# Performance work log

Measured on AMD Instinct MI355X. Metric: run time of the kernel, lower is better.

The kernel has to match this reference:

```python
import jax, jax.numpy as jnp
import numpy as np
from jax import lax

S = 2          # scale_factor
SS = S * S     # scale_factor ** 2 = groups = deform_groups
K = 3
KK = K * K
PAD = K // 2
EPS = 1e-5


def setup_inputs() -> dict:
    key = jax.random.key(0)
    k1, k2, k3, k4, k5, k6 = jax.random.split(key, 6)
    B, C, H, W = 2, 64, 128, 128
    Cin = C * SS            # 256, DCN input channels after repeat
    Cout = 64 * SS          # 256, DCN output channels
    x = jax.random.normal(k1, (B, C, H, W), jnp.float32)
    # small offset-branch weights so learned offsets stay within a few pixels
    w_offset = jax.random.normal(k2, (3 * SS * KK, Cin, K, K), jnp.float32) * 0.01
    b_offset = jax.random.normal(k3, (3 * SS * KK,), jnp.float32) * 0.01
    w_dcn = jax.random.normal(k4, (Cout, Cin // SS, K, K), jnp.float32) * (1.0 / np.sqrt((Cin // SS) * KK))
    gamma = jax.random.normal(k5, (64,), jnp.float32) * 0.1 + 1.0
    beta = jax.random.normal(k6, (64,), jnp.float32) * 0.1
    return {"x": x, "w_offset": w_offset, "b_offset": b_offset,
            "w_dcn": w_dcn, "gamma": gamma, "beta": beta}


def _deform_upsample(x, w_offset, b_offset, w_dcn, gamma, beta):
    B, C, H, W = x.shape
    xr = jnp.tile(x, (1, SS, 1, 1))            # [B, C*SS, H, W]
    Cin = C * SS
    dg = SS
    # ---- conv_offset branch (standard conv, pad=1) ----
    off = lax.conv_general_dilated(
        xr, w_offset, window_strides=(1, 1), padding=[(PAD, PAD), (PAD, PAD)],
        dimension_numbers=("NCHW", "OIHW", "NCHW"))
    off = off + b_offset[None, :, None, None]
    o1, o2, mask = jnp.split(off, 3, axis=1)
    offset = jnp.concatenate([o1, o2], axis=1).reshape(B, dg, KK, 2, H, W)
    dy = offset[:, :, :, 0]                    # [B, dg, KK, H, W]
    dx = offset[:, :, :, 1]
    mask = jax.nn.sigmoid(mask).reshape(B, dg, KK, H, W)
    # ---- deformable bilinear sampling ----
    kh = (jnp.arange(KK) // K - PAD).astype(jnp.float32)   # kernel tap row offsets
    kw = (jnp.arange(KK) % K - PAD).astype(jnp.float32)
    hh = jnp.arange(H, dtype=jnp.float32)
    ww = jnp.arange(W, dtype=jnp.float32)
    py = hh[None, :, None] + kh[:, None, None] + dy        # [B, dg, KK, H, W]
    px = ww[None, None, :] + kw[:, None, None] + dx
    y0f = jnp.floor(py)
    x0f = jnp.floor(px)
    ly = py - y0f
    lx = px - x0f
    y0 = y0f.astype(jnp.int32)
    x0 = x0f.astype(jnp.int32)
    Cg = Cin // dg
    xg = xr.reshape(B, dg, Cg, H * W)

    def gather(yi, xi):
        valid = (yi >= 0) & (yi < H) & (xi >= 0) & (xi < W)  # [B, dg, KK, H, W]
        yc = jnp.clip(yi, 0, H - 1)
        xc = jnp.clip(xi, 0, W - 1)
        idx = (yc * W + xc).reshape(B, dg, -1)               # [B, dg, KK*H*W]
        v = jax.vmap(jax.vmap(lambda xf, i: xf[:, i]))(xg, idx)  # [B, dg, Cg, KK*H*W]
        v = v.reshape(B, dg, Cg, KK, H, W)
        return v * valid[:, :, None].astype(v.dtype)

    w00 = (1 - ly) * (1 - lx)
    w01 = (1 - ly) * lx
    w10 = ly * (1 - lx)
    w11 = ly * lx
    col = (gather(y0, x0) * w00[:, :, None]
           + gather(y0, x0 + 1) * w01[:, :, None]
           + gather(y0 + 1, x0) * w10[:, :, None]
           + gather(y0 + 1, x0 + 1) * w11[:, :, None])       # [B, dg, Cg, KK, H, W]
    col = col * mask[:, :, None]
    # ---- grouped conv (groups == deform_groups, channel partitions coincide) ----
    Cout = w_dcn.shape[0]
    Cog = Cout // dg
    wg = w_dcn.reshape(dg, Cog, Cg, KK)
    y = jnp.einsum("bgcphw,gocp->bgohw", col, wg).reshape(B, Cout, H, W)
    # ---- channel reshuffle (pixel-shuffle style upsample) ----
    outc = Cout // SS
    y = y.reshape(B, S, S, outc, H, W).transpose(0, 3, 4, 1, 5, 2)
    y = y.reshape(B, outc, H * S, W * S)
    # ---- BatchNorm (batch stats, training mode) + ReLU ----
    mean = y.mean(axis=(0, 2, 3), keepdims=True)
    var = y.var(axis=(0, 2, 3), keepdims=True)
    y = (y - mean) * lax.rsqrt(var + EPS) * gamma[None, :, None, None] + beta[None, :, None, None]
    return jax.nn.relu(y)


def reference(x, w_offset, b_offset, w_dcn, gamma, beta):
    return _deform_upsample(x, w_offset, b_offset, w_dcn, gamma, beta)
```

## Files before the change

### kernel.cpp

```cpp
#include <hip/hip_runtime.h>
#include <hip/hip_bf16.h>
#include <math.h>

#define CH 64
#define HH 128
#define WW 128
#define HW 16384
#define NVALS 131072.f

#define STATS  0
#define BIAS2  256
#define WACONV 384
#define WADCN  32640
#define OACC   106368
#define XT     1875840
#define PARTS  2924416

typedef unsigned short ushort_t;
typedef unsigned int uint_t;
typedef __attribute__((ext_vector_type(8))) short bf16x8;
typedef __attribute__((ext_vector_type(4))) float f32x4;

__device__ __forceinline__ float bflo(uint_t u) { return __uint_as_float(u << 16); }
__device__ __forceinline__ float bfhi(uint_t u) { return __uint_as_float(u & 0xFFFF0000u); }
__device__ __forceinline__ float bfu(ushort_t s) { return __uint_as_float(((uint_t)s) << 16); }
__device__ __forceinline__ ushort_t f2bf(float f) {
    __hip_bfloat16 h = __float2bfloat16(f);
    return *(ushort_t*)&h;
}
__device__ __forceinline__ uint_t pack2(float lo, float hi) {
    return (uint_t)f2bf(lo) | ((uint_t)f2bf(hi) << 16);
}

__device__ __forceinline__ int off_chan(int g, int j) {
    return (j < 18) ? (g * 18 + j) : (72 + g * 9 + (j - 18));
}

__global__ void prep(const float* __restrict__ w_offset, const float* __restrict__ b_offset,
                     const float* __restrict__ w_dcn, float* __restrict__ ws) {
    int tid = blockIdx.x * 256 + threadIdx.x;
    if (tid < 64512) {
        int jp = tid & 7;
        int lane = (tid >> 3) & 63;
        int rest = tid >> 9;
        int mt = rest % 7;
        int kt = rest / 7;
        int m = mt * 16 + (lane & 15);
        int off = ((lane >> 4) << 3) + jp;
        int c = ((kt & 1) << 5) + off;
        int k = kt >> 1;
        float s = 0.f;
        if (m < 108) {
            int och = off_chan(m / 27, m % 27);
#pragma unroll
            for (int ss = 0; ss < 4; ++ss)
                s += w_offset[(och * 256 + ss * 64 + c) * 9 + k];
        }
        ((ushort_t*)(ws + WACONV))[tid] = f2bf(s);
    }
    if (tid < 147456) {
        int jp = tid & 7;
        int lane = (tid >> 3) & 63;
        int q = tid >> 9;
        int mt = q & 3;
        int kt = (q >> 2) % 18;
        int g = q / 72;
        int m = mt * 16 + (lane & 15);
        int c = ((kt & 1) << 5) + ((lane >> 4) << 3) + jp;
        int tap = kt >> 1;
        ((ushort_t*)(ws + WADCN))[tid] = f2bf(w_dcn[((g * 64 + m) * 64 + c) * 9 + tap]);
    }
    if (tid < 108) ws[BIAS2 + tid] = b_offset[off_chan(tid / 27, tid % 27)];
    if (tid < 128) ws[STATS + tid] = 0.f;
}

__global__ __launch_bounds__(256) void transpose_x(const float* __restrict__ x,
                                                   ushort_t* __restrict__ xT) {
    int b = blockIdx.x >> 8;
    int px0 = (blockIdx.x & 255) << 6;
    __shared__ float lds[64][65];
    int t = threadIdx.x;
    int lx = t & 63;
    int row = t >> 6;
    const float* xb = x + (size_t)b * CH * HW;
#pragma unroll
    for (int i = 0; i < 16; ++i) {
        int c = i * 4 + row;
        lds[c][lx] = xb[(size_t)c * HW + px0 + lx];
    }
    __syncthreads();
    ushort_t* dst = xT + ((size_t)b * HW + px0) * 64;
#pragma unroll
    for (int i = 0; i < 16; ++i) {
        int p = i * 4 + row;
        dst[(size_t)p * 64 + lx] = f2bf(lds[lx][p]);
    }
}

__global__ __launch_bounds__(256, 2) void conv_mfma(const ushort_t* __restrict__ xT,
                                                    const ushort_t* __restrict__ wA,
                                                    const float* __restrict__ biasM,
                                                    ushort_t* __restrict__ oaccb) {
    int blk = blockIdx.x;
    int b = blk >> 7;
    int tile = blk & 127;
    int th = tile >> 3, tw = tile & 7;
    int t = threadIdx.x;
    int wv = t >> 6, lane = t & 63;
    int lw = lane & 15, kg = lane >> 4;

    __shared__ ushort_t lds[180 * 72];

    const ushort_t* xTb = xT + (size_t)b * HW * 64;
    for (int rr = t; rr < 180; rr += 256) {
        int r = rr / 18, c2 = rr - r * 18;
        int hy = th * 8 + r - 1, wx = tw * 16 + c2 - 1;
        bool valid = (hy >= 0) && (hy < HH) && (wx >= 0) && (wx < WW);
        uint4* dst = (uint4*)&lds[rr * 72];
        if (valid) {
            const uint4* src = (const uint4*)(xTb + ((size_t)(hy * WW + wx)) * 64);
#pragma unroll
            for (int ch = 0; ch < 8; ++ch) dst[ch] = src[ch];
        } else {
            uint4 z; z.x = z.y = z.z = z.w = 0;
#pragma unroll
            for (int ch = 0; ch < 8; ++ch) dst[ch] = z;
        }
    }
    __syncthreads();

    f32x4 acc[7][2];
#pragma unroll
    for (int mt = 0; mt < 7; ++mt)
#pragma unroll
        for (int i = 0; i < 2; ++i)
            acc[mt][i] = (f32x4){0.f, 0.f, 0.f, 0.f};

    const bf16x8* wAv = (const bf16x8*)wA;
    for (int kt = 0; kt < 18; ++kt) {
        int k = kt >> 1;
        int dh = k / 3, dw = k - dh * 3;
        int hh = kt & 1;
        bf16x8 bfrag[2];
#pragma unroll
        for (int i = 0; i < 2; ++i) {
            int nt = wv * 2 + i;
            int rr = (nt + dh) * 18 + lw + dw;
            bfrag[i] = *(const bf16x8*)&lds[rr * 72 + ((hh << 2) + kg) * 8];
        }
        bf16x8 afrag[7];
#pragma unroll
        for (int mt = 0; mt < 7; ++mt)
            afrag[mt] = wAv[(kt * 7 + mt) * 64 + lane];
#pragma unroll
        for (int mt = 0; mt < 7; ++mt)
#pragma unroll
            for (int i = 0; i < 2; ++i)
                acc[mt][i] = __builtin_amdgcn_mfma_f32_16x16x32_bf16(
                    afrag[mt], bfrag[i], acc[mt][i], 0, 0, 0);
    }

#pragma unroll
    for (int mt = 0; mt < 7; ++mt) {
#pragma unroll
        for (int r = 0; r < 4; ++r) {
            int m = mt * 16 + (kg << 2) + r;
            if (m < 108) {
                float bia = biasM[m];
#pragma unroll
                for (int i = 0; i < 2; ++i) {
                    int hgl = th * 8 + wv * 2 + i;
                    int wgl = tw * 16 + lw;
                    oaccb[((size_t)b * 108 + m) * HW + hgl * WW + wgl] =
                        f2bf(acc[mt][i][r] + bia);
                }
            }
        }
    }
}

__global__ __launch_bounds__(256, 4) void dcn_mfma(const ushort_t* __restrict__ xT,
                                                   const ushort_t* __restrict__ oaccb,
                                                   const ushort_t* __restrict__ wA,
                                                   float* __restrict__ out) {
    int blk = blockIdx.x;
    int xcd = blk & 7;
    int b = xcd >> 2;
    int quad = xcd & 3;
    int unit = blk >> 3;
    int g = unit >> 5;
    int tl = unit & 31;
    int th = quad * 4 + (tl >> 3);
    int tw = tl & 7;
    int t = threadIdx.x;
    int wv = t >> 6, lane = t & 63;
    int lw = lane & 15, kg = lane >> 4;

    __shared__ ushort_t colLDS[128 * 72];
    __shared__ uint_t idxLDS[4][128];
    __shared__ float  wgtLDS[4][128];

    const ushort_t* xTb = xT + (size_t)b * HW * 64;

    int p1 = t & 127;
    int h1 = th * 8 + (p1 >> 4);
    int w1 = tw * 16 + (p1 & 15);
    const ushort_t* ob_in = oaccb + (size_t)(b * 4 + g) * 27 * HW + h1 * WW + w1;

    f32x4 acc[4][2];
#pragma unroll
    for (int mt = 0; mt < 4; ++mt)
#pragma unroll
        for (int i = 0; i < 2; ++i)
            acc[mt][i] = (f32x4){0.f, 0.f, 0.f, 0.f};

    const bf16x8* wAv = (const bf16x8*)wA + (size_t)g * 4608;

    for (int k = 0; k < 9; ++k) {
        if (t < 128) {
            float dy = bfu(ob_in[(size_t)(2 * k) * HW]);
            float dx = bfu(ob_in[(size_t)(2 * k + 1) * HW]);
            float mk = 1.f / (1.f + expf(-bfu(ob_in[(size_t)(18 + k) * HW])));

            float py = (float)h1 + (float)(k / 3 - 1) + dy;
            float qx = (float)w1 + (float)(k % 3 - 1) + dx;
            float y0f = floorf(py), x0f = floorf(qx);
            float ly = py - y0f, lx = qx - x0f;
            int y0 = (int)y0f, x0 = (int)x0f;
            int y1 = y0 + 1, x1 = x0 + 1;

            bool vy0 = (y0 >= 0) && (y0 < HH), vy1 = (y1 >= 0) && (y1 < HH);
            bool vx0 = (x0 >= 0) && (x0 < WW), vx1 = (x1 >= 0) && (x1 < WW);
            int yc0 = min(max(y0, 0), HH - 1), yc1 = min(max(y1, 0), HH - 1);
            int xc0 = min(max(x0, 0), WW - 1), xc1 = min(max(x1, 0), WW - 1);

            idxLDS[0][p1] = (uint_t)(yc0 * WW + xc0);
            idxLDS[1][p1] = (uint_t)(yc0 * WW + xc1);
            idxLDS[2][p1] = (uint_t)(yc1 * WW + xc0);
            idxLDS[3][p1] = (uint_t)(yc1 * WW + xc1);
            wgtLDS[0][p1] = (1.f - ly) * (1.f - lx) * mk * ((vy0 && vx0) ? 1.f : 0.f);
            wgtLDS[1][p1] = (1.f - ly) * lx * mk * ((vy0 && vx1) ? 1.f : 0.f);
            wgtLDS[2][p1] = ly * (1.f - lx) * mk * ((vy1 && vx0) ? 1.f : 0.f);
            wgtLDS[3][p1] = ly * lx * mk * ((vy1 && vx1) ? 1.f : 0.f);
        }
        __syncthreads();

        int chunk = t & 7;
#pragma unroll
        for (int iter = 0; iter < 4; ++iter) {
            int p = iter * 32 + (t >> 3);
            uint_t i00 = idxLDS[0][p], i01 = idxLDS[1][p];
            uint_t i10 = idxLDS[2][p], i11 = idxLDS[3][p];
            float w00 = wgtLDS[0][p], w01 = wgtLDS[1][p];
            float w10 = wgtLDS[2][p], w11 = wgtLDS[3][p];
            uint4 u00 = *(const uint4*)(xTb + (size_t)i00 * 64 + chunk * 8);
            uint4 u01 = *(const uint4*)(xTb + (size_t)i01 * 64 + chunk * 8);
            uint4 u10 = *(const uint4*)(xTb + (size_t)i10 * 64 + chunk * 8);
            uint4 u11 = *(const uint4*)(xTb + (size_t)i11 * 64 + chunk * 8);
            uint4 res;
#define CMB(E) pack2(w00 * bflo(u00.E) + w01 * bflo(u01.E) + w10 * bflo(u10.E) + w11 * bflo(u11.E), \
                     w00 * bfhi(u00.E) + w01 * bfhi(u01.E) + w10 * bfhi(u10.E) + w11 * bfhi(u11.E))
            res.x = CMB(x);
            res.y = CMB(y);
            res.z = CMB(z);
            res.w = CMB(w);
#undef CMB
            *(uint4*)&colLDS[p * 72 + chunk * 8] = res;
        }
        __syncthreads();

#pragma unroll
        for (int kt2 = 0; kt2 < 2; ++kt2) {
            int kt = k * 2 + kt2;
            bf16x8 bfrag[2];
#pragma unroll
            for (int i = 0; i < 2; ++i)
                bfrag[i] = *(const bf16x8*)
                    &colLDS[((wv * 2 + i) * 16 + lw) * 72 + (kt2 * 4 + kg) * 8];
            bf16x8 afrag[4];
#pragma unroll
            for (int mt = 0; mt < 4; ++mt)
                afrag[mt] = wAv[(kt * 4 + mt) * 64 + lane];
#pragma unroll
            for (int mt = 0; mt < 4; ++mt)
#pragma unroll
                for (int i = 0; i < 2; ++i)
                    acc[mt][i] = __builtin_amdgcn_mfma_f32_16x16x32_bf16(
                        afrag[mt], bfrag[i], acc[mt][i], 0, 0, 0);
        }
        __syncthreads();
    }

    int s1 = g >> 1, s2 = g & 1;
#pragma unroll
    for (int mt = 0; mt < 4; ++mt) {
#pragma unroll
        for (int i = 0; i < 2; ++i) {
            int p2 = (wv * 2 + i) * 16 + lw;
            int hg = th * 8 + (p2 >> 4);
            int wg = tw * 16 + (p2 & 15);
            float* op = out + ((size_t)b * 64 + mt * 16 + (kg << 2)) * 65536
                      + (size_t)(hg * 2 + s1) * 256 + (wg * 2 + s2);
#pragma unroll
            for (int r = 0; r < 4; ++r)
                op[(size_t)r * 65536] = acc[mt][i][r];
        }
    }
}

__global__ __launch_bounds__(256) void stats_sum(const float* __restrict__ out,
                                                 float* __restrict__ parts) {
    int o = blockIdx.x >> 2;
    int part = blockIdx.x & 3;
    int t = threadIdx.x;
    float s = 0.f, s2 = 0.f;
#pragma unroll
    for (int b = 0; b < 2; ++b) {
        const float* p = out + (size_t)b * 64 * 65536 + (size_t)o * 65536
                       + (size_t)part * 16384;
        for (int i = t * 4; i < 16384; i += 1024) {
            float4 v = *(const float4*)(p + i);
            s += v.x + v.y + v.z + v.w;
            s2 += v.x * v.x + v.y * v.y + v.z * v.z + v.w * v.w;
        }
    }
    __shared__ float red[512];
    red[t] = s;
    red[256 + t] = s2;
    __syncthreads();
#pragma unroll
    for (int m = 128; m >= 1; m >>= 1) {
        if (t < m) {
            red[t] += red[t + m];
            red[256 + t] += red[256 + t + m];
        }
        __syncthreads();
    }
    if (t == 0) {
        parts[part * 128 + o] = red[0];
        parts[part * 128 + 64 + o] = red[256];
    }
}

__global__ void finalize(const float* __restrict__ parts,
                         const float* __restrict__ gamma,
                         const float* __restrict__ beta,
                         float* __restrict__ ab) {
    int t = threadIdx.x;
    if (t < 64) {
        float s = 0.f, s2 = 0.f;
#pragma unroll
        for (int p = 0; p < 4; ++p) {
            s += parts[p * 128 + t];
            s2 += parts[p * 128 + 64 + t];
        }
        float mean = s / NVALS;
        float var = s2 / NVALS - mean * mean;
        var = fmaxf(var, 0.f);
        float a = gamma[t] * rsqrtf(var + 1e-5f);
        ab[t] = a;
        ab[64 + t] = beta[t] - mean * a;
    }
}

__global__ void norm_relu(float* __restrict__ out, const float* __restrict__ ab) {
    size_t tid = (size_t)blockIdx.x * 256 + threadIdx.x;
    size_t base = tid * 4;
    int o = (int)((base >> 16) & 63);
    float a = ab[o], bb = ab[64 + o];
    float4* p = (float4*)(out + base);
    float4 v = *p;
    v.x = fmaxf(fmaf(v.x, a, bb), 0.f);
    v.y = fmaxf(fmaf(v.y, a, bb), 0.f);
    v.z = fmaxf(fmaf(v.z, a, bb), 0.f);
    v.w = fmaxf(fmaf(v.w, a, bb), 0.f);
    *p = v;
}

extern "C" void kernel_launch(void* const* d_in, const int* in_sizes, int n_in,
                              void* d_out, int out_size, void* d_ws, size_t ws_size,
                              hipStream_t stream) {
    const float* x        = (const float*)d_in[0];
    const float* w_offset = (const float*)d_in[1];
    const float* b_offset = (const float*)d_in[2];
    const float* w_dcn    = (const float*)d_in[3];
    const float* gamma    = (const float*)d_in[4];
    const float* beta     = (const float*)d_in[5];
    float* out            = (float*)d_out;
    float* ws = (float*)d_ws;

    prep<<<576, 256, 0, stream>>>(w_offset, b_offset, w_dcn, ws);
    transpose_x<<<512, 256, 0, stream>>>(x, (ushort_t*)(ws + XT));
    conv_mfma<<<256, 256, 0, stream>>>((ushort_t*)(ws + XT), (ushort_t*)(ws + WACONV),
                                       ws + BIAS2, (ushort_t*)(ws + OACC));
    dcn_mfma<<<1024, 256, 0, stream>>>((ushort_t*)(ws + XT), (ushort_t*)(ws + OACC),
                                       (ushort_t*)(ws + WADCN), out);
    stats_sum<<<256, 256, 0, stream>>>(out, ws + PARTS);
    finalize<<<1, 64, 0, stream>>>(ws + PARTS, gamma, beta, ws + STATS + 128);
    norm_relu<<<8192, 256, 0, stream>>>(out, ws + STATS + 128);
}
```

Baseline: 105.0 us.

## Fuse BN statistics into DCN epilogue and double-buffer offset sampling setup

The DCN kernel now reduces per-channel sum and sum-of-squares from its accumulators (wave shuffles plus LDS) and writes per-block partials. A small reduce kernel then computes the BN scale and shift, replacing the separate stats pass that re-read the whole output and the single-block finalize. Sampling indices and weights for tap k+1 are computed into a second LDS buffer while tap k's MFMAs run, removing one barrier per tap. The costs are extra LDS and registers in the DCN kernel, and a 1024-way partial array that must be reduced.

Result: faster. 96.14 us (median of 2 runs) (-8.4%).

```diff
diff --git a/kernel.cpp b/kernel.cpp
--- a/kernel.cpp
+++ b/kernel.cpp
@@ -71,7 +71,6 @@
         ((ushort_t*)(ws + WADCN))[tid] = f2bf(w_dcn[((g * 64 + m) * 64 + c) * 9 + tap]);
     }
     if (tid < 108) ws[BIAS2 + tid] = b_offset[off_chan(tid / 27, tid % 27)];
-    if (tid < 128) ws[STATS + tid] = 0.f;
 }
 
 __global__ __launch_bounds__(256) void transpose_x(const float* __restrict__ x,
@@ -182,7 +181,8 @@
 __global__ __launch_bounds__(256, 4) void dcn_mfma(const ushort_t* __restrict__ xT,
                                                    const ushort_t* __restrict__ oaccb,
                                                    const ushort_t* __restrict__ wA,
-                                                   float* __restrict__ out) {
+                                                   float* __restrict__ out,
+                                                   float* __restrict__ parts) {
     int blk = blockIdx.x;
     int xcd = blk & 7;
     int b = xcd >> 2;
@@ -197,8 +197,10 @@
     int lw = lane & 15, kg = lane >> 4;
 
     __shared__ ushort_t colLDS[128 * 72];
-    __shared__ uint_t idxLDS[4][128];
-    __shared__ float  wgtLDS[4][128];
+    __shared__ uint_t idxLDS[2][4][128];
+    __shared__ float  wgtLDS[2][4][128];
+    __shared__ float  sumLDS[4][64];
+    __shared__ float  sqLDS[4][64];
 
     const ushort_t* xTb = xT + (size_t)b * HW * 64;
 
@@ -207,6 +209,31 @@
     int w1 = tw * 16 + (p1 & 15);
     const ushort_t* ob_in = oaccb + (size_t)(b * 4 + g) * 27 * HW + h1 * WW + w1;
 
+#define P1(KK, BUF)                                                               \
+    if (t < 128) {                                                                \
+        float dy = bfu(ob_in[(size_t)(2 * (KK)) * HW]);                           \
+        float dx = bfu(ob_in[(size_t)(2 * (KK) + 1) * HW]);                       \
+        float mk = 1.f / (1.f + expf(-bfu(ob_in[(size_t)(18 + (KK)) * HW])));     \
+        float py = (float)h1 + (float)((KK) / 3 - 1) + dy;                        \
+        float qx = (float)w1 + (float)((KK) % 3 - 1) + dx;                        \
+        float y0f = floorf(py), x0f = floorf(qx);                                 \
+        float ly = py - y0f, lx = qx - x0f;                                       \
+        int y0 = (int)y0f, x0 = (int)x0f;                                         \
+        int y1 = y0 + 1, x1 = x0 + 1;                                             \
+        bool vy0 = (y0 >= 0) && (y0 < HH), vy1 = (y1 >= 0) && (y1 < HH);          \
+        bool vx0 = (x0 >= 0) && (x0 < WW), vx1 = (x1 >= 0) && (x1 < WW);          \
+        int yc0 = min(max(y0, 0), HH - 1), yc1 = min(max(y1, 0), HH - 1);         \
+        int xc0 = min(max(x0, 0), WW - 1), xc1 = min(max(x1, 0), WW - 1);         \
+        idxLDS[BUF][0][p1] = (uint_t)(yc0 * WW + xc0);                            \
+        idxLDS[BUF][1][p1] = (uint_t)(yc0 * WW + xc1);                            \
+        idxLDS[BUF][2][p1] = (uint_t)(yc1 * WW + xc0);                            \
+        idxLDS[BUF][3][p1] = (uint_t)(yc1 * WW + xc1);                            \
+        wgtLDS[BUF][0][p1] = (1.f - ly) * (1.f - lx) * mk * ((vy0 && vx0) ? 1.f : 0.f); \
+        wgtLDS[BUF][1][p1] = (1.f - ly) * lx * mk * ((vy0 && vx1) ? 1.f : 0.f);   \
+        wgtLDS[BUF][2][p1] = ly * (1.f - lx) * mk * ((vy1 && vx0) ? 1.f : 0.f);   \
+        wgtLDS[BUF][3][p1] = ly * lx * mk * ((vy1 && vx1) ? 1.f : 0.f);           \
+    }
+
     f32x4 acc[4][2];
 #pragma unroll
     for (int mt = 0; mt < 4; ++mt)
@@ -216,43 +243,19 @@
 
     const bf16x8* wAv = (const bf16x8*)wA + (size_t)g * 4608;
 
+    P1(0, 0);
+    __syncthreads();
+
     for (int k = 0; k < 9; ++k) {
-        if (t < 128) {
-            float dy = bfu(ob_in[(size_t)(2 * k) * HW]);
-            float dx = bfu(ob_in[(size_t)(2 * k + 1) * HW]);
-            float mk = 1.f / (1.f + expf(-bfu(ob_in[(size_t)(18 + k) * HW])));
-
-            float py = (float)h1 + (float)(k / 3 - 1) + dy;
-            float qx = (float)w1 + (float)(k % 3 - 1) + dx;
-            float y0f = floorf(py), x0f = floorf(qx);
-            float ly = py - y0f, lx = qx - x0f;
-            int y0 = (int)y0f, x0 = (int)x0f;
-            int y1 = y0 + 1, x1 = x0 + 1;
-
-            bool vy0 = (y0 >= 0) && (y0 < HH), vy1 = (y1 >= 0) && (y1 < HH);
-            bool vx0 = (x0 >= 0) && (x0 < WW), vx1 = (x1 >= 0) && (x1 < WW);
-            int yc0 = min(max(y0, 0), HH - 1), yc1 = min(max(y1, 0), HH - 1);
-            int xc0 = min(max(x0, 0), WW - 1), xc1 = min(max(x1, 0), WW - 1);
-
-            idxLDS[0][p1] = (uint_t)(yc0 * WW + xc0);
-            idxLDS[1][p1] = (uint_t)(yc0 * WW + xc1);
-            idxLDS[2][p1] = (uint_t)(yc1 * WW + xc0);
-            idxLDS[3][p1] = (uint_t)(yc1 * WW + xc1);
-            wgtLDS[0][p1] = (1.f - ly) * (1.f - lx) * mk * ((vy0 && vx0) ? 1.f : 0.f);
-            wgtLDS[1][p1] = (1.f - ly) * lx * mk * ((vy0 && vx1) ? 1.f : 0.f);
-            wgtLDS[2][p1] = ly * (1.f - lx) * mk * ((vy1 && vx0) ? 1.f : 0.f);
-            wgtLDS[3][p1] = ly * lx * mk * ((vy1 && vx1) ? 1.f : 0.f);
-        }
-        __syncthreads();
-
+        int cur = k & 1;
         int chunk = t & 7;
 #pragma unroll
         for (int iter = 0; iter < 4; ++iter) {
             int p = iter * 32 + (t >> 3);
-            uint_t i00 = idxLDS[0][p], i01 = idxLDS[1][p];
-            uint_t i10 = idxLDS[2][p], i11 = idxLDS[3][p];
-            float w00 = wgtLDS[0][p], w01 = wgtLDS[1][p];
-            float w10 = wgtLDS[2][p], w11 = wgtLDS[3][p];
+            uint_t i00 = idxLDS[cur][0][p], i01 = idxLDS[cur][1][p];
+            uint_t i10 = idxLDS[cur][2][p], i11 = idxLDS[cur][3][p];
+            float w00 = wgtLDS[cur][0][p], w01 = wgtLDS[cur][1][p];
+            float w10 = wgtLDS[cur][2][p], w11 = wgtLDS[cur][3][p];
             uint4 u00 = *(const uint4*)(xTb + (size_t)i00 * 64 + chunk * 8);
             uint4 u01 = *(const uint4*)(xTb + (size_t)i01 * 64 + chunk * 8);
             uint4 u10 = *(const uint4*)(xTb + (size_t)i10 * 64 + chunk * 8);
@@ -269,6 +272,8 @@
         }
         __syncthreads();
 
+        if (k < 8) { P1(k + 1, cur ^ 1); }
+
 #pragma unroll
         for (int kt2 = 0; kt2 < 2; ++kt2) {
             int kt = k * 2 + kt2;
@@ -290,8 +295,9 @@
         }
         __syncthreads();
     }
-
-    int s1 = g >> 1, s2 = g & 1;
+#undef P1
+
+    int s1 = g >> 1, s2g = g & 1;
 #pragma unroll
     for (int mt = 0; mt < 4; ++mt) {
 #pragma unroll
@@ -300,29 +306,54 @@
             int hg = th * 8 + (p2 >> 4);
             int wg = tw * 16 + (p2 & 15);
             float* op = out + ((size_t)b * 64 + mt * 16 + (kg << 2)) * 65536
-                      + (size_t)(hg * 2 + s1) * 256 + (wg * 2 + s2);
+                      + (size_t)(hg * 2 + s1) * 256 + (wg * 2 + s2g);
 #pragma unroll
             for (int r = 0; r < 4; ++r)
                 op[(size_t)r * 65536] = acc[mt][i][r];
         }
     }
-}
-
-__global__ __launch_bounds__(256) void stats_sum(const float* __restrict__ out,
-                                                 float* __restrict__ parts) {
-    int o = blockIdx.x >> 2;
-    int part = blockIdx.x & 3;
+
+#pragma unroll
+    for (int mt = 0; mt < 4; ++mt) {
+#pragma unroll
+        for (int r = 0; r < 4; ++r) {
+            float a0 = acc[mt][0][r], a1 = acc[mt][1][r];
+            float s = a0 + a1;
+            float s2 = a0 * a0 + a1 * a1;
+#pragma unroll
+            for (int m = 1; m < 16; m <<= 1) {
+                s += __shfl_xor(s, m);
+                s2 += __shfl_xor(s2, m);
+            }
+            if (lw == 0) {
+                int ml = mt * 16 + (kg << 2) + r;
+                sumLDS[wv][ml] = s;
+                sqLDS[wv][ml] = s2;
+            }
+        }
+    }
+    __syncthreads();
+    if (t < 128) {
+        int o = t & 63;
+        bool isq = t >= 64;
+        float v = 0.f;
+#pragma unroll
+        for (int w2 = 0; w2 < 4; ++w2)
+            v += isq ? sqLDS[w2][o] : sumLDS[w2][o];
+        parts[(size_t)(isq ? 64 + o : o) * 1024 + blk] = v;
+    }
+}
+
+__global__ __launch_bounds__(256) void stats_reduce(const float* __restrict__ parts,
+                                                    const float* __restrict__ gamma,
+                                                    const float* __restrict__ beta,
+                                                    float* __restrict__ ab) {
+    int o = blockIdx.x;
     int t = threadIdx.x;
     float s = 0.f, s2 = 0.f;
-#pragma unroll
-    for (int b = 0; b < 2; ++b) {
-        const float* p = out + (size_t)b * 64 * 65536 + (size_t)o * 65536
-                       + (size_t)part * 16384;
-        for (int i = t * 4; i < 16384; i += 1024) {
-            float4 v = *(const float4*)(p + i);
-            s += v.x + v.y + v.z + v.w;
-            s2 += v.x * v.x + v.y * v.y + v.z * v.z + v.w * v.w;
-        }
+    for (int i = t; i < 1024; i += 256) {
+        s += parts[(size_t)o * 1024 + i];
+        s2 += parts[(size_t)(64 + o) * 1024 + i];
     }
     __shared__ float red[512];
     red[t] = s;
@@ -337,29 +368,12 @@
         __syncthreads();
     }
     if (t == 0) {
-        parts[part * 128 + o] = red[0];
-        parts[part * 128 + 64 + o] = red[256];
-    }
-}
-
-__global__ void finalize(const float* __restrict__ parts,
-                         const float* __restrict__ gamma,
-                         const float* __restrict__ beta,
-                         float* __restrict__ ab) {
-    int t = threadIdx.x;
-    if (t < 64) {
-        float s = 0.f, s2 = 0.f;
-#pragma unroll
-        for (int p = 0; p < 4; ++p) {
-            s += parts[p * 128 + t];
-            s2 += parts[p * 128 + 64 + t];
-        }
-        float mean = s / NVALS;
-        float var = s2 / NVALS - mean * mean;
+        float mean = red[0] / NVALS;
+        float var = red[256] / NVALS - mean * mean;
         var = fmaxf(var, 0.f);
-        float a = gamma[t] * rsqrtf(var + 1e-5f);
-        ab[t] = a;
-        ab[64 + t] = beta[t] - mean * a;
+        float a = gamma[o] * rsqrtf(var + 1e-5f);
+        ab[o] = a;
+        ab[64 + o] = beta[o] - mean * a;
     }
 }
 
@@ -394,8 +408,7 @@
     conv_mfma<<<256, 256, 0, stream>>>((ushort_t*)(ws + XT), (ushort_t*)(ws + WACONV),
                                        ws + BIAS2, (ushort_t*)(ws + OACC));
     dcn_mfma<<<1024, 256, 0, stream>>>((ushort_t*)(ws + XT), (ushort_t*)(ws + OACC),
-                                       (ushort_t*)(ws + WADCN), out);
-    stats_sum<<<256, 256, 0, stream>>>(out, ws + PARTS);
-    finalize<<<1, 64, 0, stream>>>(ws + PARTS, gamma, beta, ws + STATS + 128);
+                                       (ushort_t*)(ws + WADCN), out, ws + PARTS);
+    stats_reduce<<<64, 256, 0, stream>>>(ws + PARTS, gamma, beta, ws + STATS + 128);
     norm_relu<<<8192, 256, 0, stream>>>(out, ws + STATS + 128);
 }
```
